# Kernel optimization log

Measured on AMD Instinct MI355X. Metric: run time of the kernel, lower is better.

## Reference

```python
import jax, jax.numpy as jnp
import numpy as np


def setup_inputs() -> dict:
    key = jax.random.key(0)
    k1, k2, k3, k4 = jax.random.split(key, 4)
    tokens, d_in, d_out = 8192, 4096, 4096
    x = jax.random.normal(k1, (tokens, d_in), dtype=jnp.float32)
    # int8-valued weights stored as int32 for portability; values in [-128, 127]
    quantized_weights = jax.random.randint(k2, (d_out, d_in), -128, 128, dtype=jnp.int32)
    scales = jax.random.uniform(k3, (d_out,), dtype=jnp.float32) * 0.02 + 1e-4
    bias = jax.random.normal(k4, (d_out,), dtype=jnp.float32)
    return {"x": x, "quantized_weights": quantized_weights, "scales": scales, "bias": bias}


def reference(x, quantized_weights, scales, bias):
    # dequantize-on-the-fly linear: (x @ W_q^T) * scales + bias
    w = quantized_weights.astype(x.dtype)                # [out, in]
    out = jnp.einsum('ti,oi->to', x, w)                  # [tokens, out]
    out = out * scales[None, :].astype(x.dtype)
    out = out + bias.astype(x.dtype)
    return out
```

## Files before the change

### kernel.cpp

```cpp
#include <hip/hip_runtime.h>
#include <stdint.h>

#define M_TOK 8192
#define N_OUT 4096
#define K_IN  4096

#define BM 256
#define BN 256
#define BK 128
#define NT (K_IN / BK)
#define SEC 16384
#define BUF 65536

typedef int intx4 __attribute__((ext_vector_type(4)));

#define MFMAI8 __builtin_amdgcn_mfma_i32_16x16x64_i8


__device__ __forceinline__ void async_copy16(const void* g, void* l) {
    __builtin_amdgcn_global_load_lds(
        (__attribute__((address_space(1))) void*)(g),
        (__attribute__((address_space(3))) void*)(l),
        16, 0, 0);
}


__global__ void quant_x_kernel(const float* __restrict__ in,
                               int8_t* __restrict__ out,
                               float* __restrict__ sx) {
    const int row = blockIdx.x;
    const int tid = threadIdx.x;
    const float4* p = (const float4*)(in + (size_t)row * K_IN + tid * 16);
    float4 v0 = p[0], v1 = p[1], v2 = p[2], v3 = p[3];

    float m = fabsf(v0.x);
    m = fmaxf(m, fabsf(v0.y)); m = fmaxf(m, fabsf(v0.z)); m = fmaxf(m, fabsf(v0.w));
    m = fmaxf(m, fabsf(v1.x)); m = fmaxf(m, fabsf(v1.y));
    m = fmaxf(m, fabsf(v1.z)); m = fmaxf(m, fabsf(v1.w));
    m = fmaxf(m, fabsf(v2.x)); m = fmaxf(m, fabsf(v2.y));
    m = fmaxf(m, fabsf(v2.z)); m = fmaxf(m, fabsf(v2.w));
    m = fmaxf(m, fabsf(v3.x)); m = fmaxf(m, fabsf(v3.y));
    m = fmaxf(m, fabsf(v3.z)); m = fmaxf(m, fabsf(v3.w));

#pragma unroll
    for (int off = 32; off; off >>= 1) m = fmaxf(m, __shfl_xor(m, off));
    __shared__ float wmax[4];
    if ((tid & 63) == 0) wmax[tid >> 6] = m;
    __syncthreads();
    m = fmaxf(fmaxf(wmax[0], wmax[1]), fmaxf(wmax[2], wmax[3]));
    m = fmaxf(m, 1e-20f);

    const float rs = 127.0f / m;
    if (tid == 0) sx[row] = m * (1.0f / 127.0f);

    union { int4 v; int8_t c[16]; } u;
    u.c[0]  = (int8_t)__float2int_rn(v0.x * rs);
    u.c[1]  = (int8_t)__float2int_rn(v0.y * rs);
    u.c[2]  = (int8_t)__float2int_rn(v0.z * rs);
    u.c[3]  = (int8_t)__float2int_rn(v0.w * rs);
    u.c[4]  = (int8_t)__float2int_rn(v1.x * rs);
    u.c[5]  = (int8_t)__float2int_rn(v1.y * rs);
    u.c[6]  = (int8_t)__float2int_rn(v1.z * rs);
    u.c[7]  = (int8_t)__float2int_rn(v1.w * rs);
    u.c[8]  = (int8_t)__float2int_rn(v2.x * rs);
    u.c[9]  = (int8_t)__float2int_rn(v2.y * rs);
    u.c[10] = (int8_t)__float2int_rn(v2.z * rs);
    u.c[11] = (int8_t)__float2int_rn(v2.w * rs);
    u.c[12] = (int8_t)__float2int_rn(v3.x * rs);
    u.c[13] = (int8_t)__float2int_rn(v3.y * rs);
    u.c[14] = (int8_t)__float2int_rn(v3.z * rs);
    u.c[15] = (int8_t)__float2int_rn(v3.w * rs);
    ((int4*)(out + (size_t)row * K_IN))[tid] = u.v;
}


__global__ void quant_w_kernel(const int* __restrict__ in,
                               int8_t* __restrict__ out, int n16) {
    int i = blockIdx.x * 256 + threadIdx.x;
    if (i >= n16) return;
    const int4* p = (const int4*)in + (size_t)i * 4;
    int4 a = p[0], b = p[1], c = p[2], d = p[3];
    union { int4 v; int8_t q[16]; } u;
    u.q[0]  = (int8_t)a.x; u.q[1]  = (int8_t)a.y; u.q[2]  = (int8_t)a.z; u.q[3]  = (int8_t)a.w;
    u.q[4]  = (int8_t)b.x; u.q[5]  = (int8_t)b.y; u.q[6]  = (int8_t)b.z; u.q[7]  = (int8_t)b.w;
    u.q[8]  = (int8_t)c.x; u.q[9]  = (int8_t)c.y; u.q[10] = (int8_t)c.z; u.q[11] = (int8_t)c.w;
    u.q[12] = (int8_t)d.x; u.q[13] = (int8_t)d.y; u.q[14] = (int8_t)d.z; u.q[15] = (int8_t)d.w;
    ((int4*)out)[i] = u.v;
}


__global__ __launch_bounds__(512, 2)
void gemm_i8_kernel(const int8_t* __restrict__ A,
                    const int8_t* __restrict__ B,
                    const float* __restrict__ sx,
                    const float* __restrict__ scales,
                    const float* __restrict__ bias,
                    float* __restrict__ C) {
    __shared__ __align__(16) int8_t lds[2 * BUF];

    const int tid = threadIdx.x;

    const int nwg = (M_TOK / BM) * (N_OUT / BN);
    const int cpx = nwg / 8;
    const int wg  = (blockIdx.x % 8) * cpx + blockIdx.x / 8;
    const int bn  = wg & 15;
    const int bm  = wg >> 4;

    const int lane = tid & 63;
    const int wave = tid >> 6;
    const int wm   = wave >> 2;
    const int wn   = wave & 3;

    const int t8 = tid >> 3;
    const int cg = (tid & 7) ^ (t8 & 7);
    const int grow0 = 2 * t8 + (cg >> 2);
    const int gcol0 = (cg & 3) * 16;
    const int8_t* aP = A + (size_t)(bm * BM + grow0) * K_IN + gcol0;
    const int8_t* bP = B + (size_t)(bn * BN + grow0) * K_IN + gcol0;

    auto stA = [&](int tt, int s) {
        int8_t* d = &lds[(tt & 1) * BUF + s * SEC + tid * 16];
        const int8_t* g = aP + (size_t)tt * BK + s * 64;
        async_copy16(g, d);
        async_copy16(g + (size_t)128 * K_IN, d + 8192);
    };
    auto stB = [&](int tt, int s) {
        int8_t* d = &lds[(tt & 1) * BUF + 2 * SEC + s * SEC + tid * 16];
        const int8_t* g = bP + (size_t)tt * BK + s * 64;
        async_copy16(g, d);
        async_copy16(g + (size_t)128 * K_IN, d + 8192);
    };

    const int r16 = lane & 15;
    const int q   = lane >> 4;
    const int cr  = (((r16 & 1) << 2) + q) ^ ((r16 >> 1) & 7);
    const int aOff = (wm * 64 + (r16 >> 1)) * 128 + cr * 16;
    const int bOff = 2 * SEC + (wn * 32 + (r16 >> 1)) * 128 + cr * 16;

    intx4 acc[8][4] = {};
    intx4 afA[4], afB[4], bfA[4], bfB[4];

#define RD_A03(dst, base, s)                                                   \
    { _Pragma("unroll") for (int i = 0; i < 4; ++i)                            \
        dst[i] = *(const intx4*)((base) + (s) * SEC + aOff + i * 1024); }
#define RD_A47(dst, base, s)                                                   \
    { _Pragma("unroll") for (int i = 0; i < 4; ++i)                            \
        dst[i] = *(const intx4*)((base) + (s) * SEC + aOff + (4 + i) * 1024); }
#define RD_BF(dst, base, s)                                                    \
    { _Pragma("unroll") for (int j = 0; j < 4; ++j)                            \
        dst[j] = *(const intx4*)((base) + (s) * SEC + bOff + j * 1024); }
#define MM03(af, bf)                                                           \
    { __builtin_amdgcn_s_setprio(1);                                           \
      _Pragma("unroll") for (int i = 0; i < 4; ++i)                            \
          _Pragma("unroll") for (int j = 0; j < 4; ++j)                        \
              acc[i][j] = MFMAI8(af[i], bf[j], acc[i][j], 0, 0, 0);            \
      __builtin_amdgcn_s_setprio(0); }
#define MM47(af, bf)                                                           \
    { __builtin_amdgcn_s_setprio(1);                                           \
      _Pragma("unroll") for (int i = 0; i < 4; ++i)                            \
          _Pragma("unroll") for (int j = 0; j < 4; ++j)                        \
              acc[4 + i][j] = MFMAI8(af[i], bf[j], acc[4 + i][j], 0, 0, 0);    \
      __builtin_amdgcn_s_setprio(0); }
#define SBAR __builtin_amdgcn_sched_barrier(0)

    stA(0, 0); stB(0, 0); stA(0, 1); stB(0, 1);
    asm volatile("s_waitcnt vmcnt(0)" ::: "memory");
    __builtin_amdgcn_s_barrier();
    asm volatile("" ::: "memory");
    RD_A03(afA, lds, 0);
    RD_BF(bfA, lds, 0);

#pragma unroll 1
    for (int t = 0; t < NT; ++t) {
        const int8_t* Lb  = lds + (t & 1) * BUF;
        const int8_t* Lb2 = lds + ((t + 1) & 1) * BUF;
        const bool pf = (t + 1 < NT);

        if (pf) { stA(t + 1, 0); stA(t + 1, 1); }
        RD_A47(afB, Lb, 0);
        asm volatile("s_waitcnt lgkmcnt(4)" ::: "memory");
        SBAR;
        MM03(afA, bfA);

        if (pf) { stB(t + 1, 0); stB(t + 1, 1); }
        RD_A03(afA, Lb, 1);
        RD_BF(bfB, Lb, 1);
        asm volatile("s_waitcnt lgkmcnt(8)" ::: "memory");
        SBAR;
        MM47(afB, bfA);

        RD_A47(afB, Lb, 1);
        asm volatile("s_waitcnt lgkmcnt(4)" ::: "memory");
        SBAR;
        MM03(afA, bfB);

        asm volatile("s_waitcnt vmcnt(0) lgkmcnt(0)" ::: "memory");
        __builtin_amdgcn_s_barrier();
        asm volatile("" ::: "memory");
        if (pf) {
            RD_A03(afA, Lb2, 0);
            RD_BF(bfA, Lb2, 0);
        }
        SBAR;
        MM47(afB, bfB);
    }

    const int row0 = bm * BM + wm * 128 + q * 4;
    const int col0 = bn * BN + wn * 64 + r16;
    float sxv[8][4];
#pragma unroll
    for (int fr = 0; fr < 8; ++fr)
#pragma unroll
        for (int r = 0; r < 4; ++r)
            sxv[fr][r] = sx[row0 + fr * 16 + r];
#pragma unroll
    for (int fc = 0; fc < 4; ++fc) {
        const int n  = col0 + fc * 16;
        const float sc = scales[n];
        const float bi = bias[n];
#pragma unroll
        for (int fr = 0; fr < 8; ++fr) {
            const int m = row0 + fr * 16;
#pragma unroll
            for (int r = 0; r < 4; ++r)
                C[(size_t)(m + r) * N_OUT + n] =
                    (float)acc[fr][fc][r] * (sxv[fr][r] * sc) + bi;
        }
    }
}


extern "C" void kernel_launch(void* const* d_in, const int* in_sizes, int n_in,
                              void* d_out, int out_size, void* d_ws, size_t ws_size,
                              hipStream_t stream) {
    const float* x      = (const float*)d_in[0];
    const int*   wq     = (const int*)d_in[1];
    const float* scales = (const float*)d_in[2];
    const float* bias   = (const float*)d_in[3];
    float*       out    = (float*)d_out;

    int8_t* xq = (int8_t*)d_ws;
    int8_t* wb = xq + (size_t)M_TOK * K_IN;
    float*  sx = (float*)(wb + (size_t)N_OUT * K_IN);

    quant_x_kernel<<<M_TOK, 256, 0, stream>>>(x, xq, sx);
    const int nw16 = (N_OUT * K_IN) / 16;
    quant_w_kernel<<<nw16 / 256, 256, 0, stream>>>(wq, wb, nw16);

    const int grid = (M_TOK / BM) * (N_OUT / BN);
    gemm_i8_kernel<<<grid, 512, 0, stream>>>(xq, wb, sx, scales, bias, out);
}
```

Before: 187.6 us.

## Use four waves per block, each computing a 128x128 int8 tile

Shrinks the GEMM block from 512 to 256 threads, with waves in a 2x2 grid, so each wave owns a 128x128 output sub-tile instead of 128x64. This doubles the B fragments and accumulators held per wave. Each wave loads more global-to-LDS chunks per stage, and the LDS-wait counts are adjusted to match. The aim is higher register-level reuse: fewer LDS fragment reads per MFMA. The cost is much higher VGPR/AGPR pressure and only four waves per CU to hide LDS and memory latency.

```diff
diff --git a/kernel.cpp b/kernel.cpp
--- a/kernel.cpp
+++ b/kernel.cpp
@@ -89,7 +89,7 @@
 }
 
 
-__global__ __launch_bounds__(512, 2)
+__global__ __launch_bounds__(256, 1)
 void gemm_i8_kernel(const int8_t* __restrict__ A,
                     const int8_t* __restrict__ B,
                     const float* __restrict__ sx,
@@ -108,8 +108,8 @@
 
     const int lane = tid & 63;
     const int wave = tid >> 6;
-    const int wm   = wave >> 2;
-    const int wn   = wave & 3;
+    const int wm   = wave >> 1;
+    const int wn   = wave & 1;
 
     const int t8 = tid >> 3;
     const int cg = (tid & 7) ^ (t8 & 7);
@@ -121,24 +121,27 @@
     auto stA = [&](int tt, int s) {
         int8_t* d = &lds[(tt & 1) * BUF + s * SEC + tid * 16];
         const int8_t* g = aP + (size_t)tt * BK + s * 64;
-        async_copy16(g, d);
-        async_copy16(g + (size_t)128 * K_IN, d + 8192);
+#pragma unroll
+        for (int i = 0; i < 4; ++i)
+            async_copy16(g + (size_t)i * 64 * K_IN, d + i * 4096);
     };
     auto stB = [&](int tt, int s) {
         int8_t* d = &lds[(tt & 1) * BUF + 2 * SEC + s * SEC + tid * 16];
         const int8_t* g = bP + (size_t)tt * BK + s * 64;
-        async_copy16(g, d);
-        async_copy16(g + (size_t)128 * K_IN, d + 8192);
+#pragma unroll
+        for (int i = 0; i < 4; ++i)
+            async_copy16(g + (size_t)i * 64 * K_IN, d + i * 4096);
     };
 
     const int r16 = lane & 15;
     const int q   = lane >> 4;
     const int cr  = (((r16 & 1) << 2) + q) ^ ((r16 >> 1) & 7);
     const int aOff = (wm * 64 + (r16 >> 1)) * 128 + cr * 16;
-    const int bOff = 2 * SEC + (wn * 32 + (r16 >> 1)) * 128 + cr * 16;
-
-    intx4 acc[8][4] = {};
-    intx4 afA[4], afB[4], bfA[4], bfB[4];
+    const int bOff = 2 * SEC + (wn * 64 + (r16 >> 1)) * 128 + cr * 16;
+
+    intx4 acc[8][8] = {};
+    intx4 af03X[4], af47X[4], af03Y[4], af47Y[4];
+    intx4 bfX[8], bfY[8];
 
 #define RD_A03(dst, base, s)                                                   \
     { _Pragma("unroll") for (int i = 0; i < 4; ++i)                            \
@@ -146,29 +149,29 @@
 #define RD_A47(dst, base, s)                                                   \
     { _Pragma("unroll") for (int i = 0; i < 4; ++i)                            \
         dst[i] = *(const intx4*)((base) + (s) * SEC + aOff + (4 + i) * 1024); }
-#define RD_BF(dst, base, s)                                                    \
-    { _Pragma("unroll") for (int j = 0; j < 4; ++j)                            \
+#define RD_B8(dst, base, s)                                                    \
+    { _Pragma("unroll") for (int j = 0; j < 8; ++j)                            \
         dst[j] = *(const intx4*)((base) + (s) * SEC + bOff + j * 1024); }
 #define MM03(af, bf)                                                           \
     { __builtin_amdgcn_s_setprio(1);                                           \
       _Pragma("unroll") for (int i = 0; i < 4; ++i)                            \
-          _Pragma("unroll") for (int j = 0; j < 4; ++j)                        \
+          _Pragma("unroll") for (int j = 0; j < 8; ++j)                        \
               acc[i][j] = MFMAI8(af[i], bf[j], acc[i][j], 0, 0, 0);            \
       __builtin_amdgcn_s_setprio(0); }
 #define MM47(af, bf)                                                           \
     { __builtin_amdgcn_s_setprio(1);                                           \
       _Pragma("unroll") for (int i = 0; i < 4; ++i)                            \
-          _Pragma("unroll") for (int j = 0; j < 4; ++j)                        \
+          _Pragma("unroll") for (int j = 0; j < 8; ++j)                        \
               acc[4 + i][j] = MFMAI8(af[i], bf[j], acc[4 + i][j], 0, 0, 0);    \
       __builtin_amdgcn_s_setprio(0); }
 #define SBAR __builtin_amdgcn_sched_barrier(0)
 
-    stA(0, 0); stB(0, 0); stA(0, 1); stB(0, 1);
+    stA(0, 0); stA(0, 1); stB(0, 0); stB(0, 1);
     asm volatile("s_waitcnt vmcnt(0)" ::: "memory");
     __builtin_amdgcn_s_barrier();
     asm volatile("" ::: "memory");
-    RD_A03(afA, lds, 0);
-    RD_BF(bfA, lds, 0);
+    RD_A03(af03X, lds, 0);
+    RD_B8(bfX, lds, 0);
 
 #pragma unroll 1
     for (int t = 0; t < NT; ++t) {
@@ -177,36 +180,36 @@
         const bool pf = (t + 1 < NT);
 
         if (pf) { stA(t + 1, 0); stA(t + 1, 1); }
-        RD_A47(afB, Lb, 0);
+        RD_A47(af47X, Lb, 0);
         asm volatile("s_waitcnt lgkmcnt(4)" ::: "memory");
         SBAR;
-        MM03(afA, bfA);
+        MM03(af03X, bfX);
 
         if (pf) { stB(t + 1, 0); stB(t + 1, 1); }
-        RD_A03(afA, Lb, 1);
-        RD_BF(bfB, Lb, 1);
-        asm volatile("s_waitcnt lgkmcnt(8)" ::: "memory");
-        SBAR;
-        MM47(afB, bfA);
-
-        RD_A47(afB, Lb, 1);
+        RD_A03(af03Y, Lb, 1);
+        RD_B8(bfY, Lb, 1);
+        asm volatile("s_waitcnt lgkmcnt(12)" ::: "memory");
+        SBAR;
+        MM47(af47X, bfX);
+
+        RD_A47(af47Y, Lb, 1);
         asm volatile("s_waitcnt lgkmcnt(4)" ::: "memory");
         SBAR;
-        MM03(afA, bfB);
+        MM03(af03Y, bfY);
 
         asm volatile("s_waitcnt vmcnt(0) lgkmcnt(0)" ::: "memory");
         __builtin_amdgcn_s_barrier();
         asm volatile("" ::: "memory");
         if (pf) {
-            RD_A03(afA, Lb2, 0);
-            RD_BF(bfA, Lb2, 0);
+            RD_A03(af03X, Lb2, 0);
+            RD_B8(bfX, Lb2, 0);
         }
         SBAR;
-        MM47(afB, bfB);
+        MM47(af47Y, bfY);
     }
 
     const int row0 = bm * BM + wm * 128 + q * 4;
-    const int col0 = bn * BN + wn * 64 + r16;
+    const int col0 = bn * BN + wn * 128 + r16;
     float sxv[8][4];
 #pragma unroll
     for (int fr = 0; fr < 8; ++fr)
@@ -214,7 +217,7 @@
         for (int r = 0; r < 4; ++r)
             sxv[fr][r] = sx[row0 + fr * 16 + r];
 #pragma unroll
-    for (int fc = 0; fc < 4; ++fc) {
+    for (int fc = 0; fc < 8; ++fc) {
         const int n  = col0 + fc * 16;
         const float sc = scales[n];
         const float bi = bias[n];
@@ -248,5 +251,5 @@
     quant_w_kernel<<<nw16 / 256, 256, 0, stream>>>(wq, wb, nw16);
 
     const int grid = (M_TOK / BM) * (N_OUT / BN);
-    gemm_i8_kernel<<<grid, 512, 0, stream>>>(xq, wb, sx, scales, bias, out);
-}
+    gemm_i8_kernel<<<grid, 256, 0, stream>>>(xq, wb, sx, scales, bias, out);
+}
```

After: 357.6 us. +90.6%, slower.

## Switch int8 GEMM to triple-buffered LDS pipeline with K-tile of 64

Applied to the files above, without the earlier changes.

Halves the K tile from 128 to 64 and replaces the two 64 KB LDS buffers with three 32 KB buffers. Loads now run two tiles ahead of compute, and the main loop is unrolled by two with rotating buffer pointers. The aim is to hide more global-load latency, since each wait only needs the older of two in-flight stages rather than draining all loads before the barrier. The cost is twice as many workgroup barriers per unit of K, smaller MFMA batches between barriers, and more complex register and buffer rotation.

```diff
diff --git a/kernel.cpp b/kernel.cpp
--- a/kernel.cpp
+++ b/kernel.cpp
@@ -7,10 +7,10 @@
 
 #define BM 256
 #define BN 256
-#define BK 128
+#define BK 64
 #define NT (K_IN / BK)
-#define SEC 16384
-#define BUF 65536
+#define BUFS 32768
+#define BOFF 16384
 
 typedef int intx4 __attribute__((ext_vector_type(4)));
 
@@ -96,7 +96,7 @@
                     const float* __restrict__ scales,
                     const float* __restrict__ bias,
                     float* __restrict__ C) {
-    __shared__ __align__(16) int8_t lds[2 * BUF];
+    __shared__ __align__(16) int8_t lds[3 * BUFS];
 
     const int tid = threadIdx.x;
 
@@ -118,37 +118,33 @@
     const int8_t* aP = A + (size_t)(bm * BM + grow0) * K_IN + gcol0;
     const int8_t* bP = B + (size_t)(bn * BN + grow0) * K_IN + gcol0;
 
-    auto stA = [&](int tt, int s) {
-        int8_t* d = &lds[(tt & 1) * BUF + s * SEC + tid * 16];
-        const int8_t* g = aP + (size_t)tt * BK + s * 64;
-        async_copy16(g, d);
-        async_copy16(g + (size_t)128 * K_IN, d + 8192);
-    };
-    auto stB = [&](int tt, int s) {
-        int8_t* d = &lds[(tt & 1) * BUF + 2 * SEC + s * SEC + tid * 16];
-        const int8_t* g = bP + (size_t)tt * BK + s * 64;
-        async_copy16(g, d);
-        async_copy16(g + (size_t)128 * K_IN, d + 8192);
+    auto stage = [&](int8_t* d, int tt) {
+        const int8_t* ga = aP + (size_t)tt * BK;
+        async_copy16(ga, d + tid * 16);
+        async_copy16(ga + (size_t)128 * K_IN, d + 8192 + tid * 16);
+        const int8_t* gb = bP + (size_t)tt * BK;
+        async_copy16(gb, d + BOFF + tid * 16);
+        async_copy16(gb + (size_t)128 * K_IN, d + BOFF + 8192 + tid * 16);
     };
 
     const int r16 = lane & 15;
     const int q   = lane >> 4;
     const int cr  = (((r16 & 1) << 2) + q) ^ ((r16 >> 1) & 7);
     const int aOff = (wm * 64 + (r16 >> 1)) * 128 + cr * 16;
-    const int bOff = 2 * SEC + (wn * 32 + (r16 >> 1)) * 128 + cr * 16;
+    const int bOff = BOFF + (wn * 32 + (r16 >> 1)) * 128 + cr * 16;
 
     intx4 acc[8][4] = {};
-    intx4 afA[4], afB[4], bfA[4], bfB[4];
-
-#define RD_A03(dst, base, s)                                                   \
+    intx4 af03A[4], af03B[4], af47[4], bfA[4], bfB[4];
+
+#define RD_A03(dst, base)                                                      \
     { _Pragma("unroll") for (int i = 0; i < 4; ++i)                            \
-        dst[i] = *(const intx4*)((base) + (s) * SEC + aOff + i * 1024); }
-#define RD_A47(dst, base, s)                                                   \
+        dst[i] = *(const intx4*)((base) + aOff + i * 1024); }
+#define RD_A47(dst, base)                                                      \
     { _Pragma("unroll") for (int i = 0; i < 4; ++i)                            \
-        dst[i] = *(const intx4*)((base) + (s) * SEC + aOff + (4 + i) * 1024); }
-#define RD_BF(dst, base, s)                                                    \
+        dst[i] = *(const intx4*)((base) + aOff + (4 + i) * 1024); }
+#define RD_B4(dst, base)                                                       \
     { _Pragma("unroll") for (int j = 0; j < 4; ++j)                            \
-        dst[j] = *(const intx4*)((base) + (s) * SEC + bOff + j * 1024); }
+        dst[j] = *(const intx4*)((base) + bOff + j * 1024); }
 #define MM03(af, bf)                                                           \
     { __builtin_amdgcn_s_setprio(1);                                           \
       _Pragma("unroll") for (int i = 0; i < 4; ++i)                            \
@@ -163,46 +159,46 @@
       __builtin_amdgcn_s_setprio(0); }
 #define SBAR __builtin_amdgcn_sched_barrier(0)
 
-    stA(0, 0); stB(0, 0); stA(0, 1); stB(0, 1);
-    asm volatile("s_waitcnt vmcnt(0)" ::: "memory");
+#define TILE(t, af03C, bfC, af03N, bfN, Rcur, Rnxt, Rst)                       \
+    {                                                                          \
+        RD_A47(af47, Rcur);                                                    \
+        asm volatile("s_waitcnt lgkmcnt(4)" ::: "memory");                     \
+        SBAR;                                                                  \
+        MM03(af03C, bfC);                                                      \
+        if ((t) + 2 < NT) stage(Rst, (t) + 2);                                 \
+        if ((t) + 1 < NT) {                                                    \
+            if ((t) + 2 < NT)                                                  \
+                asm volatile("s_waitcnt vmcnt(4) lgkmcnt(0)" ::: "memory");    \
+            else                                                               \
+                asm volatile("s_waitcnt vmcnt(0) lgkmcnt(0)" ::: "memory");    \
+            __builtin_amdgcn_s_barrier();                                      \
+            asm volatile("" ::: "memory");                                     \
+            RD_A03(af03N, Rnxt);                                               \
+            RD_B4(bfN, Rnxt);                                                  \
+        } else {                                                               \
+            asm volatile("s_waitcnt lgkmcnt(0)" ::: "memory");                 \
+        }                                                                      \
+        SBAR;                                                                  \
+        MM47(af47, bfC);                                                       \
+    }
+
+    int8_t* r0 = lds;
+    int8_t* r1 = lds + BUFS;
+    int8_t* r2 = lds + 2 * BUFS;
+
+    stage(r0, 0);
+    stage(r1, 1);
+    asm volatile("s_waitcnt vmcnt(4)" ::: "memory");
     __builtin_amdgcn_s_barrier();
     asm volatile("" ::: "memory");
-    RD_A03(afA, lds, 0);
-    RD_BF(bfA, lds, 0);
+    RD_A03(af03A, r0);
+    RD_B4(bfA, r0);
 
 #pragma unroll 1
-    for (int t = 0; t < NT; ++t) {
-        const int8_t* Lb  = lds + (t & 1) * BUF;
-        const int8_t* Lb2 = lds + ((t + 1) & 1) * BUF;
-        const bool pf = (t + 1 < NT);
-
-        if (pf) { stA(t + 1, 0); stA(t + 1, 1); }
-        RD_A47(afB, Lb, 0);
-        asm volatile("s_waitcnt lgkmcnt(4)" ::: "memory");
-        SBAR;
-        MM03(afA, bfA);
-
-        if (pf) { stB(t + 1, 0); stB(t + 1, 1); }
-        RD_A03(afA, Lb, 1);
-        RD_BF(bfB, Lb, 1);
-        asm volatile("s_waitcnt lgkmcnt(8)" ::: "memory");
-        SBAR;
-        MM47(afB, bfA);
-
-        RD_A47(afB, Lb, 1);
-        asm volatile("s_waitcnt lgkmcnt(4)" ::: "memory");
-        SBAR;
-        MM03(afA, bfB);
-
-        asm volatile("s_waitcnt vmcnt(0) lgkmcnt(0)" ::: "memory");
-        __builtin_amdgcn_s_barrier();
-        asm volatile("" ::: "memory");
-        if (pf) {
-            RD_A03(afA, Lb2, 0);
-            RD_BF(bfA, Lb2, 0);
-        }
-        SBAR;
-        MM47(afB, bfB);
+    for (int t = 0; t < NT; t += 2) {
+        TILE(t,     af03A, bfA, af03B, bfB, r0, r1, r2)
+        TILE(t + 1, af03B, bfB, af03A, bfA, r1, r2, r0)
+        int8_t* tmp = r0; r0 = r2; r2 = r1; r1 = tmp;
     }
 
     const int row0 = bm * BM + wm * 128 + q * 4;
```

After: 198.5 us. +5.8%, slower.
